# Optimization experiments

Hardware: AMD Instinct MI355X
Metric: run time of the kernel (lower is better)

The kernel has to match this reference:

```python
import jax, jax.numpy as jnp
import numpy as np

N_QUBITS = 6
BLOCKS = 3
LATENT = 3
DIM = 1 << N_QUBITS  # 64, state-vector size
BATCH = 131072
INP_DIM = 6  # must equal N_QUBITS (repo applies linear_pre to the n_qubits-dim recon)

# Wire 0 is the most-significant qubit (PennyLane convention).
_idx = np.arange(DIM)
BITS = ((_idx[:, None] >> (N_QUBITS - 1 - np.arange(N_QUBITS))) & 1)  # (64, 6)
# Chain of CZ(k, k+1): all diagonal, fold into one sign vector per block.
CZ_SIGN = jnp.asarray(np.prod(1 - 2 * (BITS[:, :-1] * BITS[:, 1:]), axis=1).astype(np.float32))  # (64,)
Z_SIGNS = jnp.asarray((1 - 2 * BITS).astype(np.float32))  # (64, 6): <Z_k> signs per basis state


def _apply_1q(state, U, wire):
    # state: (B, 64) complex64; U: (2,2) complex64 acting on `wire`
    B = state.shape[0]
    s = state.reshape(B, 1 << wire, 2, 1 << (N_QUBITS - 1 - wire))
    s = jnp.einsum('ij,bxjy->bxiy', U, s)
    return s.reshape(B, DIM)


def _circuit(amps, weights, n_out):
    # AmplitudeEmbedding with normalize=True (x was already unit-normed in torch; idempotent)
    norm = jnp.linalg.norm(amps, axis=1, keepdims=True)
    state = (amps / norm).astype(jnp.complex64)  # (B, 64)
    for j in range(BLOCKS):
        for k in range(N_QUBITS):
            tx = weights[j, k, 0]
            tz = weights[j, k, 1]
            c = jnp.cos(0.5 * tx).astype(jnp.complex64)
            s = jnp.sin(0.5 * tx).astype(jnp.complex64)
            em = jnp.exp(-0.5j * tz).astype(jnp.complex64)
            ep = jnp.exp(0.5j * tz).astype(jnp.complex64)
            # Fused U = RZ(tz) @ RX(tx)
            U = jnp.stack([jnp.stack([em * c, -1j * em * s]),
                           jnp.stack([-1j * ep * s, ep * c])])
            state = _apply_1q(state, U, k)
        state = state * CZ_SIGN  # all CZ gates of the block, fused
    probs = state.real ** 2 + state.imag ** 2  # (B, 64)
    return probs @ Z_SIGNS[:, :n_out]  # expval(PauliZ(k)) for k < n_out


def setup_inputs() -> dict:
    key = jax.random.key(0)
    k1, k2, k3, k4, k5 = jax.random.split(key, 5)
    x = jax.random.normal(k1, (BATCH, INP_DIM), dtype=jnp.float32)
    bound = 1.0 / np.sqrt(INP_DIM)
    W_pre = jax.random.uniform(k2, (DIM, INP_DIM), minval=-bound, maxval=bound, dtype=jnp.float32)
    b_pre = jax.random.uniform(k3, (DIM,), minval=-bound, maxval=bound, dtype=jnp.float32)
    enc_w = jax.random.normal(k4, (BLOCKS, N_QUBITS, 3), dtype=jnp.float32) * 0.01
    dec_w = jax.random.normal(k5, (BLOCKS, N_QUBITS, 3), dtype=jnp.float32) * 0.01
    return {'x': x, 'W_pre': W_pre, 'b_pre': b_pre, 'enc_w': enc_w, 'dec_w': dec_w}


def reference(x, W_pre, b_pre, enc_w, dec_w):
    h = jnp.tanh(x @ W_pre.T + b_pre)                     # (B, 64)
    latent = _circuit(h, enc_w, LATENT)                    # (B, 3)
    padded = jnp.zeros((x.shape[0], DIM), jnp.float32).at[:, :LATENT].set(latent)
    recon = _circuit(padded, dec_w, N_QUBITS)              # (B, 6)
    reconstructed = jnp.tanh(recon @ W_pre.T + b_pre)      # (B, 64)
    return reconstructed, latent
```

## Files before the change

### kernel.cpp

```cpp
#include <hip/hip_runtime.h>

#define BATCH 131072

typedef float v2f __attribute__((ext_vector_type(2)));

__device__ __forceinline__ float fast_tanh(float v) {
    float e = __expf(2.0f * v);
    return 1.0f - 2.0f / (e + 1.0f);
}

template <int CTRL>
__device__ __forceinline__ float dppf(float v) {
    return __int_as_float(__builtin_amdgcn_update_dpp(
        0, __float_as_int(v), CTRL, 0xF, 0xF, true));
}
#define DPP_XOR1 0xB1
#define DPP_XOR2 0x4E

__device__ __forceinline__ v2f swap2(v2f v) { return __builtin_shufflevector(v, v, 1, 0); }

template <int MASK>
__device__ __forceinline__ void rx_pairs(v2f* zr, v2f* zi, float c, float s) {
#pragma unroll
    for (int j = 0; j < 8; ++j) {
        if (j & MASK) continue;
        int j1 = j | MASK;
        v2f ar = zr[j], ai = zi[j], br = zr[j1], bi = zi[j1];
        zr[j]  = c * ar + s * bi;
        zi[j]  = c * ai - s * br;
        zr[j1] = c * br + s * ai;
        zi[j1] = c * bi - s * ar;
    }
}

template <int CTRL>
__device__ __forceinline__ void rx_exch2(v2f* zr, v2f* zi, float c, float s) {
#pragma unroll
    for (int j = 0; j < 8; ++j) {
        v2f pr, pi;
        pr.x = dppf<CTRL>(zr[j].x);
        pr.y = dppf<CTRL>(zr[j].y);
        pi.x = dppf<CTRL>(zi[j].x);
        pi.y = dppf<CTRL>(zi[j].y);
        v2f mr = zr[j], mi = zi[j];
        zr[j] = c * mr + s * pi;
        zi[j] = c * mi - s * pr;
    }
}

__device__ __forceinline__ void enc_tail(v2f* zr, v2f* zi, const float* rx,
                                         const float* sDblk, int sub) {
    rx_pairs<2>(zr, zi, rx[2], rx[3]);
    rx_pairs<1>(zr, zi, rx[4], rx[5]);
    {
        float c = rx[6], s = rx[7];
#pragma unroll
        for (int j = 0; j < 8; ++j) {
            v2f orr = zr[j], oi = zi[j];
            zr[j] = c * orr + s * swap2(oi);
            zi[j] = c * oi - s * swap2(orr);
        }
    }
    rx_exch2<DPP_XOR2>(zr, zi, rx[8], rx[9]);
    rx_exch2<DPP_XOR1>(zr, zi, rx[10], rx[11]);
#pragma unroll
    for (int j = 0; j < 8; ++j) {
        float4 d = *(const float4*)&sDblk[(j * 4 + sub) * 4];
        v2f dr = {d.x, d.y}, di = {d.z, d.w};
        v2f orr = zr[j], oi = zi[j];
        zr[j] = dr * orr - di * oi;
        zi[j] = dr * oi + di * orr;
    }
}

__global__ __launch_bounds__(256, 4) void qae_fused(const float* __restrict__ x,
                                                    const float* __restrict__ Wp,
                                                    const float* __restrict__ bp,
                                                    const float* __restrict__ enc_w,
                                                    const float* __restrict__ dec_w,
                                                    float* __restrict__ out) {
    __shared__ __align__(16) float gt[144];
    __shared__ __align__(16) float Sr[256];
    __shared__ __align__(16) float Si[256];
    __shared__ float sA[36];
    __shared__ float sRx[36];
    __shared__ __align__(16) float sW[544];
    __shared__ __align__(16) float sB[544];
    __shared__ __align__(16) float sD[256];

    const int t = threadIdx.x;
    const int bl = t >> 2;
    const int sub = t & 3;

    const size_t b = (size_t)blockIdx.x * 64 + bl;
    const float* xp = x + b * 6;
    float2 x01 = *(const float2*)(xp);
    float2 x23 = *(const float2*)(xp + 2);
    float2 x45 = *(const float2*)(xp + 4);

    if (t < 64) {
        if (t < 18) {
            float tx = dec_w[t * 3 + 0];
            float tz = dec_w[t * 3 + 1];
            float c = cosf(0.5f * tx), s = sinf(0.5f * tx);
            float ch = cosf(0.5f * tz), sh = sinf(0.5f * tz);
            gt[t * 8 + 0] = c * ch;  gt[t * 8 + 1] = -c * sh;
            gt[t * 8 + 2] = -s * sh; gt[t * 8 + 3] = -s * ch;
            gt[t * 8 + 4] = s * sh;  gt[t * 8 + 5] = -s * ch;
            gt[t * 8 + 6] = c * ch;  gt[t * 8 + 7] = c * sh;
            float etx = enc_w[t * 3 + 0];
            float ec = cosf(0.5f * etx), es = sinf(0.5f * etx);
            if (t >= 12) {
                sRx[2 * t] = ec * ec - es * es;
                sRx[2 * t + 1] = 4.0f * ec * es;
            } else {
                sRx[2 * t] = ec;
                sRx[2 * t + 1] = es;
            }
        }
#pragma unroll
        for (int q = 0; q < 4; ++q) {
            int f = t + 64 * q;
            int r = f >> 2, c = f & 3;
            Sr[f] = (r == c && c < 3) ? 1.0f : 0.0f;
            Si[f] = 0.0f;
        }
        const int cl = t & 3;
        const int pq = t >> 2;
        for (int bb = 0; bb < 3; ++bb) {
            for (int w = 0; w < 6; ++w) {
                int g = bb * 6 + w;
                int p = 5 - w;
                float u00r = gt[g * 8 + 0], u00i = gt[g * 8 + 1];
                float u01r = gt[g * 8 + 2], u01i = gt[g * 8 + 3];
                float u10r = gt[g * 8 + 4], u10i = gt[g * 8 + 5];
                float u11r = gt[g * 8 + 6], u11i = gt[g * 8 + 7];
#pragma unroll
                for (int h = 0; h < 2; ++h) {
                    int pp = pq + 16 * h;
                    int r0 = ((pp >> p) << (p + 1)) | (pp & ((1 << p) - 1));
                    int r1 = r0 | (1 << p);
                    float ar = Sr[r0 * 4 + cl], ai = Si[r0 * 4 + cl];
                    float br = Sr[r1 * 4 + cl], bi = Si[r1 * 4 + cl];
                    Sr[r0 * 4 + cl] = u00r * ar - u00i * ai + u01r * br - u01i * bi;
                    Si[r0 * 4 + cl] = u00r * ai + u00i * ar + u01r * bi + u01i * br;
                    Sr[r1 * 4 + cl] = u10r * ar - u10i * ai + u11r * br - u11i * bi;
                    Si[r1 * 4 + cl] = u10r * ai + u10i * ar + u11r * bi + u11i * br;
                }
            }
#pragma unroll
            for (int q = 0; q < 4; ++q) {
                int f = t + 64 * q;
                int r = f >> 2;
                if (__popc(r & (r >> 1)) & 1) {
                    Sr[f] = -Sr[f];
                    Si[f] = -Si[f];
                }
            }
        }
    } else if (t < 192) {
#pragma unroll
        for (int q = 0; q < 4; ++q) {
            int f = (t - 64) + 128 * q;
            int g = f >> 4, e = f & 15;
            int j = g >> 2, su = g & 3;
            float val;
            if (e < 12)      { int row = 8 * j + su + 4 * (e & 1); val = Wp[row * 6 + (e >> 1)]; }
            else if (e < 14) { int row = 8 * j + su + 4 * (e - 12); val = bp[row]; }
            else val = 0.0f;
            sW[g * 16 + j * 4 + e] = val;
        }
    } else {
#pragma unroll
        for (int q = 0; q < 2; ++q) {
            int idx = (t - 192) + 64 * q;
            int bb = idx >> 6, r = idx & 63;
            float phi = 0.0f;
            for (int k = 0; k < 6; ++k) {
                float tz = enc_w[(bb * 6 + k) * 3 + 1];
                phi += ((r >> (5 - k)) & 1) ? 0.5f * tz : -0.5f * tz;
            }
            float sgn = (__popc(r & (r >> 1)) & 1) ? -1.0f : 1.0f;
            int su = r & 3, m = r >> 2, j = m >> 1, hm = m & 1;
            int base = ((bb * 8 + j) * 4 + su) * 4;
            sD[base + hm]     = sgn * cosf(phi);
            sD[base + 2 + hm] = sgn * sinf(phi);
        }
    }
    __syncthreads();

    if (t < 36) {
        int k = t / 6, i = t % 6;
        int d = (i < 3) ? i : ((i == 5) ? 1 : 0);
        int e = (i < 3) ? i : ((i == 3) ? 1 : 2);
        float acc = 0.0f;
        for (int r = 0; r < 64; ++r) {
            float term = Sr[r * 4 + d] * Sr[r * 4 + e] + Si[r * 4 + d] * Si[r * 4 + e];
            acc += ((r >> (5 - k)) & 1) ? -term : term;
        }
        if (i >= 3) acc *= 2.0f;
        sA[t] = acc;
    }
    __syncthreads();

    if (t < 64) {
        float w0 = Wp[t * 6 + 0], w1 = Wp[t * 6 + 1], w2 = Wp[t * 6 + 2];
        float w3 = Wp[t * 6 + 3], w4 = Wp[t * 6 + 4], w5 = Wp[t * 6 + 5];
        int basep = 8 * t + ((t >> 4) << 2);
#pragma unroll
        for (int i = 0; i < 6; ++i) {
            float acc = w0 * sA[0 * 6 + i] + w1 * sA[1 * 6 + i] + w2 * sA[2 * 6 + i]
                      + w3 * sA[3 * 6 + i] + w4 * sA[4 * 6 + i] + w5 * sA[5 * 6 + i];
            sB[basep + i] = acc;
        }
        sB[basep + 6] = bp[t];
        sB[basep + 7] = 0.0f;
    }
    __syncthreads();

    float xv[6] = {x01.x, x01.y, x23.x, x23.y, x45.x, x45.y};

    v2f zr[8], zi[8];
    v2f S2 = {0.0f, 0.0f};
#pragma unroll
    for (int j = 0; j < 8; ++j) {
        const float* wb = &sW[(j * 4 + sub) * 16 + j * 4];
        float4 c0 = *(const float4*)wb;
        float4 c1 = *(const float4*)(wb + 4);
        float4 c2 = *(const float4*)(wb + 8);
        float4 c3 = *(const float4*)(wb + 12);
        v2f a = {c3.x, c3.y};
        a += xv[0] * (v2f){c0.x, c0.y};
        a += xv[1] * (v2f){c0.z, c0.w};
        a += xv[2] * (v2f){c1.x, c1.y};
        a += xv[3] * (v2f){c1.z, c1.w};
        a += xv[4] * (v2f){c2.x, c2.y};
        a += xv[5] * (v2f){c2.z, c2.w};
        v2f th = {fast_tanh(a.x), fast_tanh(a.y)};
        zr[j] = th;
        S2 += th * th;
    }
    float S = S2.x + S2.y;
    S += dppf<DPP_XOR1>(S);
    S += dppf<DPP_XOR2>(S);
    float invS = __builtin_amdgcn_rcpf(S);

    {
        const float* rx = sRx;
        float c = rx[0], s = rx[1];
#pragma unroll
        for (int j = 0; j < 4; ++j) {
            v2f a = zr[j], b2 = zr[j + 4];
            zr[j]     = c * a;
            zi[j]     = -s * b2;
            zr[j + 4] = c * b2;
            zi[j + 4] = -s * a;
        }
        enc_tail(zr, zi, rx, sD, sub);
    }
    {
        const float* rx = sRx + 12;
        rx_pairs<4>(zr, zi, rx[0], rx[1]);
        enc_tail(zr, zi, rx, sD + 128, sub);
    }

    v2f L0 = {0, 0}, L1 = {0, 0}, L2 = {0, 0};
#pragma unroll
    for (int j = 0; j < 8; ++j) {
        v2f p = zr[j] * zr[j] + zi[j] * zi[j];
        L0 += (j & 4) ? -p : p;
        L1 += (j & 2) ? -p : p;
        L2 += (j & 1) ? -p : p;
    }
    v2f Y0 = {0, 0}, Y1 = {0, 0}, Y2 = {0, 0};
#pragma unroll
    for (int j = 0; j < 4; ++j)
        Y0 += zr[j] * zi[j | 4] - zi[j] * zr[j | 4];
#pragma unroll
    for (int j0 = 0; j0 < 8; j0 += 4)
#pragma unroll
        for (int j = j0; j < j0 + 2; ++j)
            Y1 += zr[j] * zi[j | 2] - zi[j] * zr[j | 2];
#pragma unroll
    for (int j = 0; j < 8; j += 2)
        Y2 += zr[j] * zi[j | 1] - zi[j] * zr[j | 1];

    const float* p2 = sRx + 24;
    float t0 = p2[0] * (L0.x + L0.y) + p2[1] * (Y0.x + Y0.y);
    float t1 = p2[2] * (L1.x + L1.y) + p2[3] * (Y1.x + Y1.y);
    float t2 = p2[4] * (L2.x + L2.y) + p2[5] * (Y2.x + Y2.y);
    t0 += dppf<DPP_XOR1>(t0); t0 += dppf<DPP_XOR2>(t0);
    t1 += dppf<DPP_XOR1>(t1); t1 += dppf<DPP_XOR2>(t1);
    t2 += dppf<DPP_XOR1>(t2); t2 += dppf<DPP_XOR2>(t2);
    float l0 = t0 * invS, l1 = t1 * invS, l2 = t2 * invS;

    if (sub == 0) {
        size_t lo = (size_t)BATCH * 64 + b * 3;
        out[lo]     = l0;
        out[lo + 1] = l1;
        out[lo + 2] = l2;
    }

    float q0 = l0 * l0, q1 = l1 * l1, q2 = l2 * l2;
    float invr2 = __builtin_amdgcn_rcpf(q0 + q1 + q2);
    float qh0 = q0 * invr2, qh1 = q1 * invr2, qh2 = q2 * invr2;
    float qh3 = (l0 * l1) * invr2, qh4 = (l0 * l2) * invr2, qh5 = (l1 * l2) * invr2;

    const float* bB = &sB[132 * sub];
    const size_t ob = b * 64 + 16 * sub;
#pragma unroll
    for (int ch = 0; ch < 4; ++ch) {
        float v4[4];
#pragma unroll
        for (int r = 0; r < 4; ++r) {
            int qq = ch * 4 + r;
            float4 u0 = *(const float4*)&bB[8 * qq];
            float4 u1 = *(const float4*)&bB[8 * qq + 4];
            float acc = u1.z
                      + qh0 * u0.x + qh1 * u0.y + qh2 * u0.z + qh3 * u0.w
                      + qh4 * u1.x + qh5 * u1.y;
            v4[r] = fast_tanh(acc);
        }
        float4 o = {v4[0], v4[1], v4[2], v4[3]};
        *(float4*)&out[ob + ch * 4] = o;
    }
}

extern "C" void kernel_launch(void* const* d_in, const int* in_sizes, int n_in,
                              void* d_out, int out_size, void* d_ws, size_t ws_size,
                              hipStream_t stream) {
    const float* x   = (const float*)d_in[0];
    const float* Wp  = (const float*)d_in[1];
    const float* bpv = (const float*)d_in[2];
    const float* enc = (const float*)d_in[3];
    const float* dec = (const float*)d_in[4];
    float* out = (float*)d_out;

    qae_fused<<<(BATCH * 4) / 256, 256, 0, stream>>>(x, Wp, bpv, enc, dec, out);
}
```

Baseline: 100.3 us.

## Process two batch samples per thread with packed v2f across samples

Each thread now handles two batch rows (bA and bB = bA+64), packing the two samples into the lanes of each v2f instead of packing two basis states of one sample. The per-thread state grows from 8 to 16 v2f pairs, and the weight and diagonal-phase tables are re-laid out so that one scalar coefficient multiplies both samples. The grid is halved, which spreads the per-block setup (gate tables, sA/sB precompute, syncthreads) over twice as many samples and turns coefficient loads into broadcasts. The cost is roughly double register pressure under launch_bounds(256,4), with a risk of spills or lower occupancy.

```diff
diff --git a/kernel.cpp b/kernel.cpp
--- a/kernel.cpp
+++ b/kernel.cpp
@@ -17,59 +17,49 @@
 #define DPP_XOR1 0xB1
 #define DPP_XOR2 0x4E
 
-__device__ __forceinline__ v2f swap2(v2f v) { return __builtin_shufflevector(v, v, 1, 0); }
-
 template <int MASK>
-__device__ __forceinline__ void rx_pairs(v2f* zr, v2f* zi, float c, float s) {
-#pragma unroll
-    for (int j = 0; j < 8; ++j) {
-        if (j & MASK) continue;
-        int j1 = j | MASK;
-        v2f ar = zr[j], ai = zi[j], br = zr[j1], bi = zi[j1];
-        zr[j]  = c * ar + s * bi;
-        zi[j]  = c * ai - s * br;
-        zr[j1] = c * br + s * ai;
-        zi[j1] = c * bi - s * ar;
+__device__ __forceinline__ void rx_pairs16(v2f* zr, v2f* zi, float c, float s) {
+#pragma unroll
+    for (int m = 0; m < 16; ++m) {
+        if (m & MASK) continue;
+        int m1 = m | MASK;
+        v2f ar = zr[m], ai = zi[m], br = zr[m1], bi = zi[m1];
+        zr[m]  = c * ar + s * bi;
+        zi[m]  = c * ai - s * br;
+        zr[m1] = c * br + s * ai;
+        zi[m1] = c * bi - s * ar;
     }
 }
 
 template <int CTRL>
-__device__ __forceinline__ void rx_exch2(v2f* zr, v2f* zi, float c, float s) {
-#pragma unroll
-    for (int j = 0; j < 8; ++j) {
+__device__ __forceinline__ void rx_exch16(v2f* zr, v2f* zi, float c, float s) {
+#pragma unroll
+    for (int m = 0; m < 16; ++m) {
         v2f pr, pi;
-        pr.x = dppf<CTRL>(zr[j].x);
-        pr.y = dppf<CTRL>(zr[j].y);
-        pi.x = dppf<CTRL>(zi[j].x);
-        pi.y = dppf<CTRL>(zi[j].y);
-        v2f mr = zr[j], mi = zi[j];
-        zr[j] = c * mr + s * pi;
-        zi[j] = c * mi - s * pr;
-    }
-}
-
-__device__ __forceinline__ void enc_tail(v2f* zr, v2f* zi, const float* rx,
-                                         const float* sDblk, int sub) {
-    rx_pairs<2>(zr, zi, rx[2], rx[3]);
-    rx_pairs<1>(zr, zi, rx[4], rx[5]);
-    {
-        float c = rx[6], s = rx[7];
-#pragma unroll
-        for (int j = 0; j < 8; ++j) {
-            v2f orr = zr[j], oi = zi[j];
-            zr[j] = c * orr + s * swap2(oi);
-            zi[j] = c * oi - s * swap2(orr);
-        }
-    }
-    rx_exch2<DPP_XOR2>(zr, zi, rx[8], rx[9]);
-    rx_exch2<DPP_XOR1>(zr, zi, rx[10], rx[11]);
-#pragma unroll
-    for (int j = 0; j < 8; ++j) {
-        float4 d = *(const float4*)&sDblk[(j * 4 + sub) * 4];
-        v2f dr = {d.x, d.y}, di = {d.z, d.w};
-        v2f orr = zr[j], oi = zi[j];
-        zr[j] = dr * orr - di * oi;
-        zi[j] = dr * oi + di * orr;
+        pr.x = dppf<CTRL>(zr[m].x);
+        pr.y = dppf<CTRL>(zr[m].y);
+        pi.x = dppf<CTRL>(zi[m].x);
+        pi.y = dppf<CTRL>(zi[m].y);
+        v2f mr = zr[m], mi = zi[m];
+        zr[m] = c * mr + s * pi;
+        zi[m] = c * mi - s * pr;
+    }
+}
+
+__device__ __forceinline__ void enc_tail16(v2f* zr, v2f* zi, const float* rx,
+                                           const float* sDblk, int sub) {
+    rx_pairs16<4>(zr, zi, rx[2], rx[3]);
+    rx_pairs16<2>(zr, zi, rx[4], rx[5]);
+    rx_pairs16<1>(zr, zi, rx[6], rx[7]);
+    rx_exch16<DPP_XOR2>(zr, zi, rx[8], rx[9]);
+    rx_exch16<DPP_XOR1>(zr, zi, rx[10], rx[11]);
+    const float2* dp = (const float2*)sDblk;
+#pragma unroll
+    for (int m = 0; m < 16; ++m) {
+        float2 d = dp[m * 4 + sub];
+        v2f orr = zr[m], oi = zi[m];
+        zr[m] = d.x * orr - d.y * oi;
+        zi[m] = d.x * oi + d.y * orr;
     }
 }
 
@@ -84,19 +74,24 @@
     __shared__ __align__(16) float Si[256];
     __shared__ float sA[36];
     __shared__ float sRx[36];
-    __shared__ __align__(16) float sW[544];
+    __shared__ __align__(16) float sW2[512];
     __shared__ __align__(16) float sB[544];
-    __shared__ __align__(16) float sD[256];
+    __shared__ __align__(16) float sD2[256];
 
     const int t = threadIdx.x;
     const int bl = t >> 2;
     const int sub = t & 3;
 
-    const size_t b = (size_t)blockIdx.x * 64 + bl;
-    const float* xp = x + b * 6;
-    float2 x01 = *(const float2*)(xp);
-    float2 x23 = *(const float2*)(xp + 2);
-    float2 x45 = *(const float2*)(xp + 4);
+    const size_t bA = (size_t)blockIdx.x * 128 + bl;
+    const size_t bB = bA + 64;
+    const float* xpA = x + bA * 6;
+    const float* xpB = x + bB * 6;
+    float2 a01 = *(const float2*)(xpA);
+    float2 a23 = *(const float2*)(xpA + 2);
+    float2 a45 = *(const float2*)(xpA + 4);
+    float2 b01 = *(const float2*)(xpB);
+    float2 b23 = *(const float2*)(xpB + 2);
+    float2 b45 = *(const float2*)(xpB + 4);
 
     if (t < 64) {
         if (t < 18) {
@@ -162,13 +157,12 @@
 #pragma unroll
         for (int q = 0; q < 4; ++q) {
             int f = (t - 64) + 128 * q;
-            int g = f >> 4, e = f & 15;
-            int j = g >> 2, su = g & 3;
+            int row = f >> 3, e = f & 7;
             float val;
-            if (e < 12)      { int row = 8 * j + su + 4 * (e & 1); val = Wp[row * 6 + (e >> 1)]; }
-            else if (e < 14) { int row = 8 * j + su + 4 * (e - 12); val = bp[row]; }
-            else val = 0.0f;
-            sW[g * 16 + j * 4 + e] = val;
+            if (e < 6)       val = Wp[row * 6 + e];
+            else if (e == 6) val = bp[row];
+            else             val = 0.0f;
+            sW2[f] = val;
         }
     } else {
 #pragma unroll
@@ -181,10 +175,10 @@
                 phi += ((r >> (5 - k)) & 1) ? 0.5f * tz : -0.5f * tz;
             }
             float sgn = (__popc(r & (r >> 1)) & 1) ? -1.0f : 1.0f;
-            int su = r & 3, m = r >> 2, j = m >> 1, hm = m & 1;
-            int base = ((bb * 8 + j) * 4 + su) * 4;
-            sD[base + hm]     = sgn * cosf(phi);
-            sD[base + 2 + hm] = sgn * sinf(phi);
+            int m = r >> 2, su = r & 3;
+            int base = bb * 128 + (m * 4 + su) * 2;
+            sD2[base]     = sgn * cosf(phi);
+            sD2[base + 1] = sgn * sinf(phi);
         }
     }
     __syncthreads();
@@ -218,111 +212,127 @@
     }
     __syncthreads();
 
-    float xv[6] = {x01.x, x01.y, x23.x, x23.y, x45.x, x45.y};
-
-    v2f zr[8], zi[8];
+    v2f xv[6];
+    xv[0] = (v2f){a01.x, b01.x}; xv[1] = (v2f){a01.y, b01.y};
+    xv[2] = (v2f){a23.x, b23.x}; xv[3] = (v2f){a23.y, b23.y};
+    xv[4] = (v2f){a45.x, b45.x}; xv[5] = (v2f){a45.y, b45.y};
+
+    v2f zr[16], zi[16];
     v2f S2 = {0.0f, 0.0f};
 #pragma unroll
-    for (int j = 0; j < 8; ++j) {
-        const float* wb = &sW[(j * 4 + sub) * 16 + j * 4];
+    for (int m = 0; m < 16; ++m) {
+        const float* wb = &sW2[(4 * m + sub) * 8];
         float4 c0 = *(const float4*)wb;
         float4 c1 = *(const float4*)(wb + 4);
-        float4 c2 = *(const float4*)(wb + 8);
-        float4 c3 = *(const float4*)(wb + 12);
-        v2f a = {c3.x, c3.y};
-        a += xv[0] * (v2f){c0.x, c0.y};
-        a += xv[1] * (v2f){c0.z, c0.w};
-        a += xv[2] * (v2f){c1.x, c1.y};
-        a += xv[3] * (v2f){c1.z, c1.w};
-        a += xv[4] * (v2f){c2.x, c2.y};
-        a += xv[5] * (v2f){c2.z, c2.w};
+        v2f a = {c1.z, c1.z};
+        a += c0.x * xv[0];
+        a += c0.y * xv[1];
+        a += c0.z * xv[2];
+        a += c0.w * xv[3];
+        a += c1.x * xv[4];
+        a += c1.y * xv[5];
         v2f th = {fast_tanh(a.x), fast_tanh(a.y)};
-        zr[j] = th;
+        zr[m] = th;
         S2 += th * th;
     }
-    float S = S2.x + S2.y;
-    S += dppf<DPP_XOR1>(S);
-    S += dppf<DPP_XOR2>(S);
-    float invS = __builtin_amdgcn_rcpf(S);
+    S2.x += dppf<DPP_XOR1>(S2.x); S2.x += dppf<DPP_XOR2>(S2.x);
+    S2.y += dppf<DPP_XOR1>(S2.y); S2.y += dppf<DPP_XOR2>(S2.y);
+    v2f invS = {__builtin_amdgcn_rcpf(S2.x), __builtin_amdgcn_rcpf(S2.y)};
 
     {
         const float* rx = sRx;
         float c = rx[0], s = rx[1];
 #pragma unroll
-        for (int j = 0; j < 4; ++j) {
-            v2f a = zr[j], b2 = zr[j + 4];
-            zr[j]     = c * a;
-            zi[j]     = -s * b2;
-            zr[j + 4] = c * b2;
-            zi[j + 4] = -s * a;
-        }
-        enc_tail(zr, zi, rx, sD, sub);
+        for (int m = 0; m < 8; ++m) {
+            v2f a = zr[m], b2 = zr[m + 8];
+            zr[m]     = c * a;
+            zi[m]     = -s * b2;
+            zr[m + 8] = c * b2;
+            zi[m + 8] = -s * a;
+        }
+        enc_tail16(zr, zi, rx, sD2, sub);
     }
     {
         const float* rx = sRx + 12;
-        rx_pairs<4>(zr, zi, rx[0], rx[1]);
-        enc_tail(zr, zi, rx, sD + 128, sub);
+        rx_pairs16<8>(zr, zi, rx[0], rx[1]);
+        enc_tail16(zr, zi, rx, sD2 + 128, sub);
     }
 
     v2f L0 = {0, 0}, L1 = {0, 0}, L2 = {0, 0};
 #pragma unroll
-    for (int j = 0; j < 8; ++j) {
-        v2f p = zr[j] * zr[j] + zi[j] * zi[j];
-        L0 += (j & 4) ? -p : p;
-        L1 += (j & 2) ? -p : p;
-        L2 += (j & 1) ? -p : p;
+    for (int m = 0; m < 16; ++m) {
+        v2f p = zr[m] * zr[m] + zi[m] * zi[m];
+        L0 += (m & 8) ? -p : p;
+        L1 += (m & 4) ? -p : p;
+        L2 += (m & 2) ? -p : p;
     }
     v2f Y0 = {0, 0}, Y1 = {0, 0}, Y2 = {0, 0};
 #pragma unroll
-    for (int j = 0; j < 4; ++j)
-        Y0 += zr[j] * zi[j | 4] - zi[j] * zr[j | 4];
-#pragma unroll
-    for (int j0 = 0; j0 < 8; j0 += 4)
-#pragma unroll
-        for (int j = j0; j < j0 + 2; ++j)
-            Y1 += zr[j] * zi[j | 2] - zi[j] * zr[j | 2];
-#pragma unroll
-    for (int j = 0; j < 8; j += 2)
-        Y2 += zr[j] * zi[j | 1] - zi[j] * zr[j | 1];
+    for (int m = 0; m < 8; ++m)
+        Y0 += zr[m] * zi[m | 8] - zi[m] * zr[m | 8];
+#pragma unroll
+    for (int m = 0; m < 16; ++m) {
+        if (!(m & 4)) Y1 += zr[m] * zi[m | 4] - zi[m] * zr[m | 4];
+    }
+#pragma unroll
+    for (int m = 0; m < 16; ++m) {
+        if (!(m & 2)) Y2 += zr[m] * zi[m | 2] - zi[m] * zr[m | 2];
+    }
 
     const float* p2 = sRx + 24;
-    float t0 = p2[0] * (L0.x + L0.y) + p2[1] * (Y0.x + Y0.y);
-    float t1 = p2[2] * (L1.x + L1.y) + p2[3] * (Y1.x + Y1.y);
-    float t2 = p2[4] * (L2.x + L2.y) + p2[5] * (Y2.x + Y2.y);
-    t0 += dppf<DPP_XOR1>(t0); t0 += dppf<DPP_XOR2>(t0);
-    t1 += dppf<DPP_XOR1>(t1); t1 += dppf<DPP_XOR2>(t1);
-    t2 += dppf<DPP_XOR1>(t2); t2 += dppf<DPP_XOR2>(t2);
-    float l0 = t0 * invS, l1 = t1 * invS, l2 = t2 * invS;
+    v2f t0 = p2[0] * L0 + p2[1] * Y0;
+    v2f t1 = p2[2] * L1 + p2[3] * Y1;
+    v2f t2 = p2[4] * L2 + p2[5] * Y2;
+    t0.x += dppf<DPP_XOR1>(t0.x); t0.x += dppf<DPP_XOR2>(t0.x);
+    t0.y += dppf<DPP_XOR1>(t0.y); t0.y += dppf<DPP_XOR2>(t0.y);
+    t1.x += dppf<DPP_XOR1>(t1.x); t1.x += dppf<DPP_XOR2>(t1.x);
+    t1.y += dppf<DPP_XOR1>(t1.y); t1.y += dppf<DPP_XOR2>(t1.y);
+    t2.x += dppf<DPP_XOR1>(t2.x); t2.x += dppf<DPP_XOR2>(t2.x);
+    t2.y += dppf<DPP_XOR1>(t2.y); t2.y += dppf<DPP_XOR2>(t2.y);
+    v2f l0 = t0 * invS, l1 = t1 * invS, l2 = t2 * invS;
 
     if (sub == 0) {
-        size_t lo = (size_t)BATCH * 64 + b * 3;
-        out[lo]     = l0;
-        out[lo + 1] = l1;
-        out[lo + 2] = l2;
-    }
-
-    float q0 = l0 * l0, q1 = l1 * l1, q2 = l2 * l2;
-    float invr2 = __builtin_amdgcn_rcpf(q0 + q1 + q2);
-    float qh0 = q0 * invr2, qh1 = q1 * invr2, qh2 = q2 * invr2;
-    float qh3 = (l0 * l1) * invr2, qh4 = (l0 * l2) * invr2, qh5 = (l1 * l2) * invr2;
-
-    const float* bB = &sB[132 * sub];
-    const size_t ob = b * 64 + 16 * sub;
+        size_t loA = (size_t)BATCH * 64 + bA * 3;
+        size_t loB = (size_t)BATCH * 64 + bB * 3;
+        out[loA]     = l0.x;
+        out[loA + 1] = l1.x;
+        out[loA + 2] = l2.x;
+        out[loB]     = l0.y;
+        out[loB + 1] = l1.y;
+        out[loB + 2] = l2.y;
+    }
+
+    v2f q0 = l0 * l0, q1 = l1 * l1, q2 = l2 * l2;
+    v2f r2 = q0 + q1 + q2;
+    v2f invr2 = {__builtin_amdgcn_rcpf(r2.x), __builtin_amdgcn_rcpf(r2.y)};
+    v2f qh0 = q0 * invr2, qh1 = q1 * invr2, qh2 = q2 * invr2;
+    v2f qh3 = (l0 * l1) * invr2, qh4 = (l0 * l2) * invr2, qh5 = (l1 * l2) * invr2;
+
+    const float* bB2 = &sB[132 * sub];
+    const size_t obA = bA * 64 + 16 * sub;
+    const size_t obB = bB * 64 + 16 * sub;
 #pragma unroll
     for (int ch = 0; ch < 4; ++ch) {
-        float v4[4];
+        float vA[4], vB[4];
 #pragma unroll
         for (int r = 0; r < 4; ++r) {
             int qq = ch * 4 + r;
-            float4 u0 = *(const float4*)&bB[8 * qq];
-            float4 u1 = *(const float4*)&bB[8 * qq + 4];
-            float acc = u1.z
-                      + qh0 * u0.x + qh1 * u0.y + qh2 * u0.z + qh3 * u0.w
-                      + qh4 * u1.x + qh5 * u1.y;
-            v4[r] = fast_tanh(acc);
-        }
-        float4 o = {v4[0], v4[1], v4[2], v4[3]};
-        *(float4*)&out[ob + ch * 4] = o;
+            float4 u0 = *(const float4*)&bB2[8 * qq];
+            float4 u1 = *(const float4*)&bB2[8 * qq + 4];
+            v2f acc = {u1.z, u1.z};
+            acc += u0.x * qh0;
+            acc += u0.y * qh1;
+            acc += u0.z * qh2;
+            acc += u0.w * qh3;
+            acc += u1.x * qh4;
+            acc += u1.y * qh5;
+            vA[r] = fast_tanh(acc.x);
+            vB[r] = fast_tanh(acc.y);
+        }
+        float4 oA = {vA[0], vA[1], vA[2], vA[3]};
+        float4 oB = {vB[0], vB[1], vB[2], vB[3]};
+        *(float4*)&out[obA + ch * 4] = oA;
+        *(float4*)&out[obB + ch * 4] = oB;
     }
 }
 
@@ -336,5 +346,5 @@
     const float* dec = (const float*)d_in[4];
     float* out = (float*)d_out;
 
-    qae_fused<<<(BATCH * 4) / 256, 256, 0, stream>>>(x, Wp, bpv, enc, dec, out);
-}
+    qae_fused<<<BATCH / 128, 256, 0, stream>>>(x, Wp, bpv, enc, dec, out);
+}
```

Measured after the change: 100.7 us. No clear change (+0.4%).
